# Performance work log

Measured on AMD Instinct MI355X. Metric: run time of the kernel, lower is better.

## Reference

```python
import jax, jax.numpy as jnp
import numpy as np

N = 50000      # nodes
E = 600000     # edges (avg degree 12)
D_IN = 16      # node_input_size
D = 128        # hidden_size
H = 4          # num_heads
DH = D // H
L = 4          # message_passing_num
D_FF = 512     # 4*hidden FFN expansion
D_OUT = 3      # output_size


def setup_inputs() -> dict:
    key = jax.random.key(0)
    ks = iter(jax.random.split(key, 32))
    def w(shape, fan_in):
        return jax.random.normal(next(ks), shape, jnp.float32) / np.float32(np.sqrt(fan_in))
    return {
        "features": jax.random.normal(next(ks), (N, D_IN), jnp.float32),
        "senders": jax.random.randint(next(ks), (E,), 0, N),
        "receivers": jax.random.randint(next(ks), (E,), 0, N),
        "enc_w1": w((D_IN, D), D_IN), "enc_b1": jnp.zeros((D,), jnp.float32),
        "enc_w2": w((D, D), D),       "enc_b2": jnp.zeros((D,), jnp.float32),
        "wq": w((L, D, D), D), "wk": w((L, D, D), D),
        "wv": w((L, D, D), D), "wo": w((L, D, D), D),
        "ln1_s": jnp.ones((L, D), jnp.float32), "ln1_b": jnp.zeros((L, D), jnp.float32),
        "ffn_w1": w((L, D, D_FF), D), "ffn_b1": jnp.zeros((L, D_FF), jnp.float32),
        "ffn_w2": w((L, D_FF, D), D_FF), "ffn_b2": jnp.zeros((L, D), jnp.float32),
        "ln2_s": jnp.ones((L, D), jnp.float32), "ln2_b": jnp.zeros((L, D), jnp.float32),
        "dec_w1": w((D, D_OUT), D), "dec_b1": jnp.zeros((D_OUT,), jnp.float32),
        "dec_w2": w((D_OUT, D_OUT), D_OUT), "dec_b2": jnp.zeros((D_OUT,), jnp.float32),
    }


def _ln(x, s, b):
    mu = x.mean(-1, keepdims=True)
    var = ((x - mu) ** 2).mean(-1, keepdims=True)
    return (x - mu) * jax.lax.rsqrt(var + 1e-5) * s + b


def _graph_mha(x, senders, receivers, wq, wk, wv, wo):
    # Adjacency-masked attention done sparsely over the edge list
    # (equivalent to softmax over the BCOO adjacency pattern).
    n = x.shape[0]
    q = (x @ wq).reshape(n, H, DH)
    k = (x @ wk).reshape(n, H, DH)
    v = (x @ wv).reshape(n, H, DH)
    scores = (q[receivers] * k[senders]).sum(-1) / np.float32(np.sqrt(DH))  # [E,H]
    m = jax.ops.segment_max(scores, receivers, num_segments=n)             # [N,H]
    m = jnp.where(jnp.isfinite(m), m, 0.0)
    a = jnp.exp(scores - m[receivers])                                      # [E,H]
    denom = jax.ops.segment_sum(a, receivers, num_segments=n)              # [N,H]
    msg = jax.ops.segment_sum(a[:, :, None] * v[senders], receivers, num_segments=n)  # [N,H,DH]
    out = (msg / (denom[:, :, None] + 1e-9)).reshape(n, D)
    return out @ wo


def reference(features, senders, receivers,
              enc_w1, enc_b1, enc_w2, enc_b2,
              wq, wk, wv, wo, ln1_s, ln1_b,
              ffn_w1, ffn_b1, ffn_w2, ffn_b2, ln2_s, ln2_b,
              dec_w1, dec_b1, dec_w2, dec_b2):
    # encode
    x = jnp.maximum(features @ enc_w1 + enc_b1, 0.0) @ enc_w2 + enc_b2     # [N,D]
    # process: L pre-LN sparse-attention transformer blocks
    for l in range(L):
        h = _ln(x, ln1_s[l], ln1_b[l])
        x = x + _graph_mha(h, senders, receivers, wq[l], wk[l], wv[l], wo[l])
        h = _ln(x, ln2_s[l], ln2_b[l])
        x = x + jnp.maximum(h @ ffn_w1[l] + ffn_b1[l], 0.0) @ ffn_w2[l] + ffn_b2[l]
    # decode
    return jnp.maximum(x @ dec_w1 + dec_b1, 0.0) @ dec_w2 + dec_b2         # [N,D_OUT]
```

## Files before the change

### kernel.cpp

```cpp
#include <hip/hip_runtime.h>
#include <hip/hip_bf16.h>
#include <math.h>

#define D     128
#define NHEAD 4
#define DH    32
#define DFF   512
#define DIN   16
#define MAXDEG 64
#define TN    16

typedef __attribute__((ext_vector_type(8))) short bf16x8;
typedef __attribute__((ext_vector_type(4))) float f32x4;
typedef __hip_bfloat16 bf16;

#define QSCALE_L2E 0.2550348838f

#define AP 132
#define BM 64

__global__ void k_zero_int(int* p, int n) {
    int i = blockIdx.x * blockDim.x + threadIdx.x;
    if (i < n) p[i] = 0;
}

__global__ void k_fill(const int* __restrict__ recv, const int* __restrict__ senders,
                       int* __restrict__ deg, int* __restrict__ eid, int E) {
    int e = blockIdx.x * blockDim.x + threadIdx.x;
    if (e >= E) return;
    int r = recv[e];
    int pos = atomicAdd(&deg[r], 1);
    if (pos < MAXDEG) eid[r * MAXDEG + pos] = senders[e];
}

__global__ void k_wt(const float* __restrict__ wq, const float* __restrict__ wk,
                     const float* __restrict__ wv, const float* __restrict__ wo,
                     const float* __restrict__ w1, const float* __restrict__ w2,
                     const float* __restrict__ encw2,
                     bf16* __restrict__ wqkvT, bf16* __restrict__ woT,
                     bf16* __restrict__ w1T, bf16* __restrict__ w2T,
                     bf16* __restrict__ encw2T) {
    int r = blockIdx.y;
    const float* src; bf16* dst; int K, Nout;
    if (r < 12) {
        int l = r / 3, sel = r % 3;
        src = (sel == 0 ? wq : sel == 1 ? wk : wv) + (size_t)l * D * D;
        dst = wqkvT + (size_t)l * 3 * D * D + (size_t)sel * D * D;
        K = D; Nout = D;
    } else if (r < 16) {
        int l = r - 12;
        src = wo + (size_t)l * D * D; dst = woT + (size_t)l * D * D; K = D; Nout = D;
    } else if (r < 20) {
        int l = r - 16;
        src = w1 + (size_t)l * D * DFF; dst = w1T + (size_t)l * D * DFF; K = D; Nout = DFF;
    } else if (r < 24) {
        int l = r - 20;
        src = w2 + (size_t)l * DFF * D; dst = w2T + (size_t)l * DFF * D; K = DFF; Nout = D;
    } else {
        src = encw2; dst = encw2T; K = D; Nout = D;
    }
    int total = K * Nout;
    int i = blockIdx.x * blockDim.x + threadIdx.x;
    if (i >= total) return;
    int k = i / Nout, j = i % Nout;
    dst[(size_t)j * K + k] = __float2bfloat16(src[i]);
}

__device__ __forceinline__ void load_afrag(const bf16* A, int arow, int quad,
                                           int N, bf16x8* afr) {
    const bf16* ab = A + (size_t)arow * D + quad * 8;
#pragma unroll
    for (int i = 0; i < 4; i++) {
        uint4 v = make_uint4(0u, 0u, 0u, 0u);
        if (arow < N) v = *(const uint4*)(ab + i * 32);
        afr[i] = *(bf16x8*)&v;
    }
}

template<int OP>
__global__ __launch_bounds__(256) void k_gemm(
        const bf16* __restrict__ A, const bf16* __restrict__ Bt,
        const float* __restrict__ bias,
        const float* __restrict__ lns, const float* __restrict__ lnb,
        float* x, bf16* outB, int N) {
    __shared__ alignas(16) bf16 Wsm[128][AP];
    int m0 = blockIdx.x * BM;
    int t = threadIdx.x;
    int wave = t >> 6, lane = t & 63;
    int quad = lane >> 4, l16 = lane & 15;
    int wm = wave * 16;

    bf16x8 afr[4];
    load_afrag(A, m0 + wm + l16, quad, N, afr);
#pragma unroll
    for (int it = 0; it < 8; it++) {
        int ci = it * 256 + t;
        int rr = ci >> 4, cc = (ci & 15) * 8;
        *(uint4*)&Wsm[rr][cc] = *(const uint4*)(Bt + (size_t)rr * D + cc);
    }
    __syncthreads();

    f32x4 acc[8];
#pragma unroll
    for (int j = 0; j < 8; j++) acc[j] = (f32x4){0.f, 0.f, 0.f, 0.f};
#pragma unroll
    for (int i = 0; i < 4; i++) {
#pragma unroll
        for (int j = 0; j < 8; j++) {
            bf16x8 bfr = *(const bf16x8*)&Wsm[j * 16 + l16][i * 32 + quad * 8];
            acc[j] = __builtin_amdgcn_mfma_f32_16x16x32_bf16(afr[i], bfr, acc[j], 0, 0, 0);
        }
    }

    int rowb = m0 + wm + quad * 4;
    float bv[8];
    if (OP == 5) {
#pragma unroll
        for (int j = 0; j < 8; j++) bv[j] = bias[j * 16 + l16];
    }
#pragma unroll
    for (int j = 0; j < 8; j++) {
        int col = j * 16 + l16;
#pragma unroll
        for (int r = 0; r < 4; r++) {
            int gr = rowb + r;
            if (gr >= N) continue;
            float val = acc[j][r];
            if (OP == 5) val += bv[j];
            if (OP == 2) val += x[(size_t)gr * D + col];
            acc[j][r] = val;
        }
    }
    float lsv[8], lbv[8];
#pragma unroll
    for (int j = 0; j < 8; j++) {
        lsv[j] = lns[j * 16 + l16];
        lbv[j] = lnb[j * 16 + l16];
    }
#pragma unroll
    for (int r = 0; r < 4; r++) {
        float s1 = 0.f, s2 = 0.f;
#pragma unroll
        for (int j = 0; j < 8; j++) {
            float v = acc[j][r];
            s1 += v; s2 += v * v;
        }
        s1 += __shfl_xor(s1, 1, 64);  s2 += __shfl_xor(s2, 1, 64);
        s1 += __shfl_xor(s1, 2, 64);  s2 += __shfl_xor(s2, 2, 64);
        s1 += __shfl_xor(s1, 4, 64);  s2 += __shfl_xor(s2, 4, 64);
        s1 += __shfl_xor(s1, 8, 64);  s2 += __shfl_xor(s2, 8, 64);
        float mu = s1 * (1.f / 128.f);
        float var = s2 * (1.f / 128.f) - mu * mu;
        float rinv = rsqrtf(fmaxf(var, 0.f) + 1e-5f);
        int gr = rowb + r;
        if (gr >= N) continue;
#pragma unroll
        for (int j = 0; j < 8; j++) {
            int col = j * 16 + l16;
            float v = acc[j][r];
            x[(size_t)gr * D + col] = v;
            outB[(size_t)gr * D + col] =
                __float2bfloat16((v - mu) * rinv * lsv[j] + lbv[j]);
        }
    }
}

__global__ __launch_bounds__(256) void k_qkv(
        const bf16* __restrict__ hb, const bf16* __restrict__ wqkvT,
        bf16* __restrict__ qb, bf16* __restrict__ kvb, int N) {
    __shared__ alignas(16) bf16 Wsm[128][AP];
    int m0 = blockIdx.x * BM;
    int t = threadIdx.x;
    int wave = t >> 6, lane = t & 63;
    int quad = lane >> 4, l16 = lane & 15;
    int wm = wave * 16;

    bf16x8 afr[4];
    load_afrag(hb, m0 + wm + l16, quad, N, afr);

    for (int y = 0; y < 3; y++) {
        const bf16* W = wqkvT + (size_t)y * D * D;
#pragma unroll
        for (int it = 0; it < 8; it++) {
            int ci = it * 256 + t;
            int rr = ci >> 4, cc = (ci & 15) * 8;
            *(uint4*)&Wsm[rr][cc] = *(const uint4*)(W + (size_t)rr * D + cc);
        }
        __syncthreads();

        f32x4 acc[8];
#pragma unroll
        for (int j = 0; j < 8; j++) acc[j] = (f32x4){0.f, 0.f, 0.f, 0.f};
#pragma unroll
        for (int i = 0; i < 4; i++) {
#pragma unroll
            for (int j = 0; j < 8; j++) {
                bf16x8 bfr = *(const bf16x8*)&Wsm[j * 16 + l16][i * 32 + quad * 8];
                acc[j] = __builtin_amdgcn_mfma_f32_16x16x32_bf16(afr[i], bfr, acc[j], 0, 0, 0);
            }
        }
        int rowb = m0 + wm + quad * 4;
#pragma unroll
        for (int j = 0; j < 8; j++) {
            int col = j * 16 + l16;
#pragma unroll
            for (int r = 0; r < 4; r++) {
                int gr = rowb + r;
                if (gr >= N) continue;
                float val = acc[j][r];
                if (y == 0) qb[(size_t)gr * D + col] = __float2bfloat16(val * QSCALE_L2E);
                else kvb[((size_t)gr * D + col) * 2 + (y - 1)] = __float2bfloat16(val);
            }
        }
        if (y < 2) __syncthreads();
    }
}

template<bool DOLN>
__global__ __launch_bounds__(256) void k_ffn(
        const bf16* __restrict__ hb, const bf16* __restrict__ w1T,
        const float* __restrict__ b1,
        const bf16* __restrict__ w2T, const float* __restrict__ b2,
        const float* __restrict__ lns, const float* __restrict__ lnb,
        float* x, bf16* outB, int N) {
    __shared__ alignas(16) bf16 Wsm[128][AP];
    __shared__ alignas(16) bf16 Hsm[64][AP];
    int m0 = blockIdx.x * 64;
    int t = threadIdx.x;
    int wave = t >> 6, lane = t & 63;
    int quad = lane >> 4, l16 = lane & 15;
    int wm = wave * 16;

    bf16x8 afr[4];
    load_afrag(hb, m0 + wm + l16, quad, N, afr);
#pragma unroll
    for (int it = 0; it < 8; it++) {
        int ci = it * 256 + t;
        int rr = ci >> 4, cc = (ci & 15) * 8;
        *(uint4*)&Wsm[rr][cc] = *(const uint4*)(w1T + (size_t)rr * D + cc);
    }
    __syncthreads();

    f32x4 acc2[8];
#pragma unroll
    for (int j = 0; j < 8; j++) acc2[j] = (f32x4){0.f, 0.f, 0.f, 0.f};

    for (int c = 0; c < 4; c++) {
        f32x4 accP[8];
#pragma unroll
        for (int j = 0; j < 8; j++) accP[j] = (f32x4){0.f, 0.f, 0.f, 0.f};
#pragma unroll
        for (int i = 0; i < 4; i++) {
#pragma unroll
            for (int j = 0; j < 8; j++) {
                bf16x8 bfr = *(const bf16x8*)&Wsm[j * 16 + l16][i * 32 + quad * 8];
                accP[j] = __builtin_amdgcn_mfma_f32_16x16x32_bf16(afr[i], bfr, accP[j], 0, 0, 0);
            }
        }
        __syncthreads();
#pragma unroll
        for (int it = 0; it < 8; it++) {
            int ci = it * 256 + t;
            int rr = ci >> 4, cc = (ci & 15) * 8;
            *(uint4*)&Wsm[rr][cc] = *(const uint4*)(w2T + (size_t)rr * DFF + c * 128 + cc);
        }
        {
            float bv[8];
#pragma unroll
            for (int j = 0; j < 8; j++) bv[j] = b1[c * 128 + j * 16 + l16];
            int rw = wm + quad * 4;
#pragma unroll
            for (int j = 0; j < 8; j++) {
                int col = j * 16 + l16;
#pragma unroll
                for (int r = 0; r < 4; r++)
                    Hsm[rw + r][col] = __float2bfloat16(fmaxf(accP[j][r] + bv[j], 0.f));
            }
        }
        __syncthreads();
#pragma unroll
        for (int ks = 0; ks < 4; ks++) {
            bf16x8 af2 = *(const bf16x8*)&Hsm[wm + l16][ks * 32 + quad * 8];
#pragma unroll
            for (int j = 0; j < 8; j++) {
                bf16x8 bfr = *(const bf16x8*)&Wsm[j * 16 + l16][ks * 32 + quad * 8];
                acc2[j] = __builtin_amdgcn_mfma_f32_16x16x32_bf16(af2, bfr, acc2[j], 0, 0, 0);
            }
        }
        if (c < 3) {
            __syncthreads();
#pragma unroll
            for (int it = 0; it < 8; it++) {
                int ci = it * 256 + t;
                int rr = ci >> 4, cc = (ci & 15) * 8;
                *(uint4*)&Wsm[rr][cc] =
                    *(const uint4*)(w1T + (size_t)((c + 1) * 128 + rr) * D + cc);
            }
            __syncthreads();
        }
    }

    int rowb = m0 + wm + quad * 4;
    float bv[8];
#pragma unroll
    for (int j = 0; j < 8; j++) bv[j] = b2[j * 16 + l16];
#pragma unroll
    for (int j = 0; j < 8; j++) {
        int col = j * 16 + l16;
#pragma unroll
        for (int r = 0; r < 4; r++) {
            int gr = rowb + r;
            if (gr >= N) continue;
            acc2[j][r] += bv[j] + x[(size_t)gr * D + col];
        }
    }
    if (!DOLN) {
#pragma unroll
        for (int j = 0; j < 8; j++) {
            int col = j * 16 + l16;
#pragma unroll
            for (int r = 0; r < 4; r++) {
                int gr = rowb + r;
                if (gr < N) x[(size_t)gr * D + col] = acc2[j][r];
            }
        }
        return;
    }
    float lsv[8], lbv[8];
#pragma unroll
    for (int j = 0; j < 8; j++) {
        lsv[j] = lns[j * 16 + l16];
        lbv[j] = lnb[j * 16 + l16];
    }
#pragma unroll
    for (int r = 0; r < 4; r++) {
        float s1 = 0.f, s2 = 0.f;
#pragma unroll
        for (int j = 0; j < 8; j++) {
            float v = acc2[j][r];
            s1 += v; s2 += v * v;
        }
        s1 += __shfl_xor(s1, 1, 64);  s2 += __shfl_xor(s2, 1, 64);
        s1 += __shfl_xor(s1, 2, 64);  s2 += __shfl_xor(s2, 2, 64);
        s1 += __shfl_xor(s1, 4, 64);  s2 += __shfl_xor(s2, 4, 64);
        s1 += __shfl_xor(s1, 8, 64);  s2 += __shfl_xor(s2, 8, 64);
        float mu = s1 * (1.f / 128.f);
        float var = s2 * (1.f / 128.f) - mu * mu;
        float rinv = rsqrtf(fmaxf(var, 0.f) + 1e-5f);
        int gr = rowb + r;
        if (gr >= N) continue;
#pragma unroll
        for (int j = 0; j < 8; j++) {
            int col = j * 16 + l16;
            float v = acc2[j][r];
            x[(size_t)gr * D + col] = v;
            outB[(size_t)gr * D + col] = __float2bfloat16((v - mu) * rinv * lsv[j] + lbv[j]);
        }
    }
}

__global__ void k_enc1(const float* __restrict__ feat,
                       const float* __restrict__ w1, const float* __restrict__ b1,
                       bf16* __restrict__ hb, int N) {
    __shared__ float fsh[TN][DIN];
    int n0 = blockIdx.x * TN;
    int j = threadIdx.x;
    int nvalid = min(TN, N - n0);
    for (int idx = j; idx < TN * DIN; idx += 128) {
        int n = idx / DIN, i = idx % DIN;
        fsh[n][i] = (n < nvalid) ? feat[(n0 + n) * DIN + i] : 0.f;
    }
    __syncthreads();
    float bb = b1[j];
#pragma unroll
    for (int n = 0; n < TN; n++) {
        float a = bb;
#pragma unroll
        for (int i = 0; i < DIN; i++) a += fsh[n][i] * w1[i * D + j];
        if (n < nvalid) hb[(size_t)(n0 + n) * D + j] = __float2bfloat16(fmaxf(a, 0.f));
    }
}

__global__ __launch_bounds__(128) void k_attn(
        const bf16* __restrict__ qb, const uint* __restrict__ kvb,
        const int* __restrict__ deg, const int* __restrict__ eid,
        bf16* __restrict__ out, int N) {
    __shared__ float sl[32], sa[32][4];
    int r = blockIdx.x;
    int t = threadIdx.x;
    int wave = t >> 6, lane = t & 63;
    int g = lane & 7;
    int h = (lane >> 3) & 3;
    int slot = wave * 2 + (lane >> 5);
    int d0 = h * 32 + g * 4;
    uint2 qw = *(const uint2*)(qb + (size_t)r * D + d0);
    float4 qv;
    qv.x = __uint_as_float(qw.x << 16);
    qv.y = __uint_as_float(qw.x & 0xFFFF0000u);
    qv.z = __uint_as_float(qw.y << 16);
    qv.w = __uint_as_float(qw.y & 0xFFFF0000u);
    int cnt = min(deg[r], MAXDEG);
    const int* row = eid + (size_t)r * MAXDEG;
    float l = 0.f, a0 = 0.f, a1 = 0.f, a2 = 0.f, a3 = 0.f;
    for (int base = 0; base < cnt; base += 8) {
        int eiA = base + slot, eiB = base + 4 + slot;
        bool vA = eiA < cnt, vB = eiB < cnt;
        int sA = vA ? row[eiA] : 0;
        int sB = vB ? row[eiB] : 0;
        uint4 wA = *(const uint4*)(kvb + (size_t)sA * D + d0);
        uint4 wB = *(const uint4*)(kvb + (size_t)sB * D + d0);
        {
            float k0 = __uint_as_float(wA.x << 16), v0 = __uint_as_float(wA.x & 0xFFFF0000u);
            float k1 = __uint_as_float(wA.y << 16), v1 = __uint_as_float(wA.y & 0xFFFF0000u);
            float k2 = __uint_as_float(wA.z << 16), v2 = __uint_as_float(wA.z & 0xFFFF0000u);
            float k3 = __uint_as_float(wA.w << 16), v3 = __uint_as_float(wA.w & 0xFFFF0000u);
            float p = qv.x * k0 + qv.y * k1 + qv.z * k2 + qv.w * k3;
            p += __shfl_xor(p, 1, 64);
            p += __shfl_xor(p, 2, 64);
            p += __shfl_xor(p, 4, 64);
            float e = vA ? exp2f(p) : 0.f;
            l += e;
            a0 += e * v0; a1 += e * v1; a2 += e * v2; a3 += e * v3;
        }
        {
            float k0 = __uint_as_float(wB.x << 16), v0 = __uint_as_float(wB.x & 0xFFFF0000u);
            float k1 = __uint_as_float(wB.y << 16), v1 = __uint_as_float(wB.y & 0xFFFF0000u);
            float k2 = __uint_as_float(wB.z << 16), v2 = __uint_as_float(wB.z & 0xFFFF0000u);
            float k3 = __uint_as_float(wB.w << 16), v3 = __uint_as_float(wB.w & 0xFFFF0000u);
            float p = qv.x * k0 + qv.y * k1 + qv.z * k2 + qv.w * k3;
            p += __shfl_xor(p, 1, 64);
            p += __shfl_xor(p, 2, 64);
            p += __shfl_xor(p, 4, 64);
            float e = vB ? exp2f(p) : 0.f;
            l += e;
            a0 += e * v0; a1 += e * v1; a2 += e * v2; a3 += e * v3;
        }
    }
    l  += __shfl_xor(l, 32, 64);
    a0 += __shfl_xor(a0, 32, 64);
    a1 += __shfl_xor(a1, 32, 64);
    a2 += __shfl_xor(a2, 32, 64);
    a3 += __shfl_xor(a3, 32, 64);
    if (wave == 1 && lane < 32) {
        sl[lane] = l;
        sa[lane][0] = a0; sa[lane][1] = a1; sa[lane][2] = a2; sa[lane][3] = a3;
    }
    __syncthreads();
    if (wave == 0 && lane < 32) {
        l += sl[lane];
        float inv = 1.f / (l + 1e-9f);
        bf16 o[4];
        o[0] = __float2bfloat16((a0 + sa[lane][0]) * inv);
        o[1] = __float2bfloat16((a1 + sa[lane][1]) * inv);
        o[2] = __float2bfloat16((a2 + sa[lane][2]) * inv);
        o[3] = __float2bfloat16((a3 + sa[lane][3]) * inv);
        *(uint2*)(out + (size_t)r * D + d0) = *(uint2*)o;
    }
}

__global__ void k_decode(const float* __restrict__ x,
                         const float* __restrict__ w1, const float* __restrict__ b1,
                         const float* __restrict__ w2, const float* __restrict__ b2,
                         float* __restrict__ out, int N) {
    int node = blockIdx.x * 4 + (threadIdx.x >> 6);
    int lane = threadIdx.x & 63;
    if (node >= N) return;
    float a0 = x[(size_t)node * D + lane], a1 = x[(size_t)node * D + lane + 64];
    float acc0 = a0 * w1[lane * 3 + 0] + a1 * w1[(lane + 64) * 3 + 0];
    float acc1 = a0 * w1[lane * 3 + 1] + a1 * w1[(lane + 64) * 3 + 1];
    float acc2 = a0 * w1[lane * 3 + 2] + a1 * w1[(lane + 64) * 3 + 2];
#pragma unroll
    for (int m = 32; m >= 1; m >>= 1) {
        acc0 += __shfl_xor(acc0, m, 64);
        acc1 += __shfl_xor(acc1, m, 64);
        acc2 += __shfl_xor(acc2, m, 64);
    }
    if (lane == 0) {
        float t0 = fmaxf(acc0 + b1[0], 0.f);
        float t1 = fmaxf(acc1 + b1[1], 0.f);
        float t2 = fmaxf(acc2 + b1[2], 0.f);
        for (int o = 0; o < 3; o++)
            out[(size_t)node * 3 + o] =
                t0 * w2[0 * 3 + o] + t1 * w2[1 * 3 + o] + t2 * w2[2 * 3 + o] + b2[o];
    }
}

extern "C" void kernel_launch(void* const* d_in, const int* in_sizes, int n_in,
                              void* d_out, int out_size, void* d_ws, size_t ws_size,
                              hipStream_t stream) {
    const float* feat    = (const float*)d_in[0];
    const int*   senders = (const int*)d_in[1];
    const int*   recv    = (const int*)d_in[2];
    const float* enc_w1  = (const float*)d_in[3];
    const float* enc_b1  = (const float*)d_in[4];
    const float* enc_w2  = (const float*)d_in[5];
    const float* enc_b2  = (const float*)d_in[6];
    const float* wq      = (const float*)d_in[7];
    const float* wk      = (const float*)d_in[8];
    const float* wv      = (const float*)d_in[9];
    const float* wo      = (const float*)d_in[10];
    const float* ln1_s   = (const float*)d_in[11];
    const float* ln1_b   = (const float*)d_in[12];
    const float* ffn_w1  = (const float*)d_in[13];
    const float* ffn_b1  = (const float*)d_in[14];
    const float* ffn_w2  = (const float*)d_in[15];
    const float* ffn_b2  = (const float*)d_in[16];
    const float* ln2_s   = (const float*)d_in[17];
    const float* ln2_b   = (const float*)d_in[18];
    const float* dec_w1  = (const float*)d_in[19];
    const float* dec_b1  = (const float*)d_in[20];
    const float* dec_w2  = (const float*)d_in[21];
    const float* dec_b2  = (const float*)d_in[22];

    int N = in_sizes[0] / DIN;
    int E = in_sizes[1];

    char* p = (char*)d_ws;
    float* x   = (float*)p;  p += (size_t)N * D * 4;
    bf16*  qb  = (bf16*)p;   p += (size_t)N * D * 2;
    bf16*  kvb = (bf16*)p;   p += (size_t)N * D * 2 * 2;
    bf16*  hb  = (bf16*)p;   p += (size_t)N * D * 2;
    int* deg   = (int*)p;    p += (size_t)N * 4;
    int* eid   = (int*)p;    p += (size_t)N * MAXDEG * 4;
    bf16* wqkvT  = (bf16*)p; p += (size_t)4 * 3 * D * D * 2;
    bf16* woT    = (bf16*)p; p += (size_t)4 * D * D * 2;
    bf16* w1T    = (bf16*)p; p += (size_t)4 * D * DFF * 2;
    bf16* w2T    = (bf16*)p; p += (size_t)4 * DFF * D * 2;
    bf16* encw2T = (bf16*)p; p += (size_t)D * D * 2;

    int gm = (N + BM - 1) / BM;

    k_wt<<<dim3(256, 25), 256, 0, stream>>>(wq, wk, wv, wo, ffn_w1, ffn_w2, enc_w2,
                                            wqkvT, woT, w1T, w2T, encw2T);
    k_zero_int<<<(N + 255) / 256, 256, 0, stream>>>(deg, N);
    k_fill<<<(E + 255) / 256, 256, 0, stream>>>(recv, senders, deg, eid, E);
    k_enc1<<<(N + TN - 1) / TN, 128, 0, stream>>>(feat, enc_w1, enc_b1, hb, N);
    k_gemm<5><<<gm, 256, 0, stream>>>(hb, encw2T, enc_b2, ln1_s, ln1_b, x, hb, N);

    for (int l = 0; l < 4; l++) {
        k_qkv<<<gm, 256, 0, stream>>>(hb, wqkvT + (size_t)l * 3 * D * D, qb, kvb, N);
        k_attn<<<N, 128, 0, stream>>>(qb, (const uint*)kvb, deg, eid, hb, N);
        k_gemm<2><<<gm, 256, 0, stream>>>(hb, woT + (size_t)l * D * D,
                                          nullptr, ln2_s + l * D, ln2_b + l * D,
                                          x, hb, N);
        if (l < 3)
            k_ffn<true><<<gm, 256, 0, stream>>>(hb, w1T + (size_t)l * D * DFF,
                                                ffn_b1 + l * DFF,
                                                w2T + (size_t)l * DFF * D, ffn_b2 + l * D,
                                                ln1_s + (l + 1) * D, ln1_b + (l + 1) * D,
                                                x, hb, N);
        else
            k_ffn<false><<<gm, 256, 0, stream>>>(hb, w1T + (size_t)l * D * DFF,
                                                 ffn_b1 + l * DFF,
                                                 w2T + (size_t)l * DFF * D, ffn_b2 + l * D,
                                                 nullptr, nullptr, x, nullptr, N);
    }
    k_decode<<<(N + 3) / 4, 256, 0, stream>>>(x, dec_w1, dec_b1, dec_w2, dec_b2,
                                              (float*)d_out, N);
}
```

Before: 761.0 us.

## Fuse output projection, residual and LN2 into the FFN kernel

Merges the attention output-projection GEMM (plus residual add and second LayerNorm) into the FFN kernel, so the post-attention residual stays in registers and the normalized activations go through shared memory instead of global memory. This removes one kernel launch per layer and one global write and read of x and hb per layer. In exchange the fused kernel holds an extra accumulator array in registers, which may reduce occupancy, and the encoder GEMM is specialized into its own non-template kernel.

```diff
diff --git a/kernel.cpp b/kernel.cpp
--- a/kernel.cpp
+++ b/kernel.cpp
@@ -77,8 +77,7 @@
     }
 }
 
-template<int OP>
-__global__ __launch_bounds__(256) void k_gemm(
+__global__ __launch_bounds__(256) void k_gemm5(
         const bf16* __restrict__ A, const bf16* __restrict__ Bt,
         const float* __restrict__ bias,
         const float* __restrict__ lns, const float* __restrict__ lnb,
@@ -113,30 +112,17 @@
     }
 
     int rowb = m0 + wm + quad * 4;
-    float bv[8];
-    if (OP == 5) {
-#pragma unroll
-        for (int j = 0; j < 8; j++) bv[j] = bias[j * 16 + l16];
-    }
+    float bv[8], lsv[8], lbv[8];
 #pragma unroll
     for (int j = 0; j < 8; j++) {
-        int col = j * 16 + l16;
-#pragma unroll
-        for (int r = 0; r < 4; r++) {
-            int gr = rowb + r;
-            if (gr >= N) continue;
-            float val = acc[j][r];
-            if (OP == 5) val += bv[j];
-            if (OP == 2) val += x[(size_t)gr * D + col];
-            acc[j][r] = val;
-        }
-    }
-    float lsv[8], lbv[8];
-#pragma unroll
-    for (int j = 0; j < 8; j++) {
+        bv[j]  = bias[j * 16 + l16];
         lsv[j] = lns[j * 16 + l16];
         lbv[j] = lnb[j * 16 + l16];
     }
+#pragma unroll
+    for (int j = 0; j < 8; j++)
+#pragma unroll
+        for (int r = 0; r < 4; r++) acc[j][r] += bv[j];
 #pragma unroll
     for (int r = 0; r < 4; r++) {
         float s1 = 0.f, s2 = 0.f;
@@ -217,9 +203,10 @@
 }
 
 template<bool DOLN>
-__global__ __launch_bounds__(256) void k_ffn(
-        const bf16* __restrict__ hb, const bf16* __restrict__ w1T,
-        const float* __restrict__ b1,
+__global__ __launch_bounds__(256) void k_wo_ffn(
+        const bf16* __restrict__ ha, const bf16* __restrict__ woT,
+        const float* __restrict__ ln2s, const float* __restrict__ ln2b,
+        const bf16* __restrict__ w1T, const float* __restrict__ b1,
         const bf16* __restrict__ w2T, const float* __restrict__ b2,
         const float* __restrict__ lns, const float* __restrict__ lnb,
         float* x, bf16* outB, int N) {
@@ -230,16 +217,82 @@
     int wave = t >> 6, lane = t & 63;
     int quad = lane >> 4, l16 = lane & 15;
     int wm = wave * 16;
+    int rowb = m0 + wm + quad * 4;
 
     bf16x8 afr[4];
-    load_afrag(hb, m0 + wm + l16, quad, N, afr);
+    load_afrag(ha, m0 + wm + l16, quad, N, afr);
+#pragma unroll
+    for (int it = 0; it < 8; it++) {
+        int ci = it * 256 + t;
+        int rr = ci >> 4, cc = (ci & 15) * 8;
+        *(uint4*)&Wsm[rr][cc] = *(const uint4*)(woT + (size_t)rr * D + cc);
+    }
+    __syncthreads();
+
+    f32x4 accW[8];
+#pragma unroll
+    for (int j = 0; j < 8; j++) accW[j] = (f32x4){0.f, 0.f, 0.f, 0.f};
+#pragma unroll
+    for (int i = 0; i < 4; i++) {
+#pragma unroll
+        for (int j = 0; j < 8; j++) {
+            bf16x8 bfr = *(const bf16x8*)&Wsm[j * 16 + l16][i * 32 + quad * 8];
+            accW[j] = __builtin_amdgcn_mfma_f32_16x16x32_bf16(afr[i], bfr, accW[j], 0, 0, 0);
+        }
+    }
+    __syncthreads();
+
 #pragma unroll
     for (int it = 0; it < 8; it++) {
         int ci = it * 256 + t;
         int rr = ci >> 4, cc = (ci & 15) * 8;
         *(uint4*)&Wsm[rr][cc] = *(const uint4*)(w1T + (size_t)rr * D + cc);
     }
+#pragma unroll
+    for (int j = 0; j < 8; j++) {
+        int col = j * 16 + l16;
+#pragma unroll
+        for (int r = 0; r < 4; r++) {
+            int gr = rowb + r;
+            if (gr < N) accW[j][r] += x[(size_t)gr * D + col];
+        }
+    }
+    {
+        float l2s[8], l2b[8];
+#pragma unroll
+        for (int j = 0; j < 8; j++) {
+            l2s[j] = ln2s[j * 16 + l16];
+            l2b[j] = ln2b[j * 16 + l16];
+        }
+#pragma unroll
+        for (int r = 0; r < 4; r++) {
+            float s1 = 0.f, s2 = 0.f;
+#pragma unroll
+            for (int j = 0; j < 8; j++) {
+                float v = accW[j][r];
+                s1 += v; s2 += v * v;
+            }
+            s1 += __shfl_xor(s1, 1, 64);  s2 += __shfl_xor(s2, 1, 64);
+            s1 += __shfl_xor(s1, 2, 64);  s2 += __shfl_xor(s2, 2, 64);
+            s1 += __shfl_xor(s1, 4, 64);  s2 += __shfl_xor(s2, 4, 64);
+            s1 += __shfl_xor(s1, 8, 64);  s2 += __shfl_xor(s2, 8, 64);
+            float mu = s1 * (1.f / 128.f);
+            float var = s2 * (1.f / 128.f) - mu * mu;
+            float rinv = rsqrtf(fmaxf(var, 0.f) + 1e-5f);
+            int rw = wm + quad * 4 + r;
+#pragma unroll
+            for (int j = 0; j < 8; j++) {
+                int col = j * 16 + l16;
+                Hsm[rw][col] = __float2bfloat16(
+                    (accW[j][r] - mu) * rinv * l2s[j] + l2b[j]);
+            }
+        }
+    }
     __syncthreads();
+
+#pragma unroll
+    for (int i = 0; i < 4; i++)
+        afr[i] = *(const bf16x8*)&Hsm[wm + l16][i * 32 + quad * 8];
 
     f32x4 acc2[8];
 #pragma unroll
@@ -300,20 +353,14 @@
         }
     }
 
-    int rowb = m0 + wm + quad * 4;
     float bv[8];
 #pragma unroll
     for (int j = 0; j < 8; j++) bv[j] = b2[j * 16 + l16];
 #pragma unroll
-    for (int j = 0; j < 8; j++) {
-        int col = j * 16 + l16;
-#pragma unroll
-        for (int r = 0; r < 4; r++) {
-            int gr = rowb + r;
-            if (gr >= N) continue;
-            acc2[j][r] += bv[j] + x[(size_t)gr * D + col];
-        }
-    }
+    for (int j = 0; j < 8; j++)
+#pragma unroll
+        for (int r = 0; r < 4; r++)
+            acc2[j][r] += accW[j][r] + bv[j];
     if (!DOLN) {
 #pragma unroll
         for (int j = 0; j < 8; j++) {
@@ -535,25 +582,23 @@
     k_zero_int<<<(N + 255) / 256, 256, 0, stream>>>(deg, N);
     k_fill<<<(E + 255) / 256, 256, 0, stream>>>(recv, senders, deg, eid, E);
     k_enc1<<<(N + TN - 1) / TN, 128, 0, stream>>>(feat, enc_w1, enc_b1, hb, N);
-    k_gemm<5><<<gm, 256, 0, stream>>>(hb, encw2T, enc_b2, ln1_s, ln1_b, x, hb, N);
+    k_gemm5<<<gm, 256, 0, stream>>>(hb, encw2T, enc_b2, ln1_s, ln1_b, x, hb, N);
 
     for (int l = 0; l < 4; l++) {
         k_qkv<<<gm, 256, 0, stream>>>(hb, wqkvT + (size_t)l * 3 * D * D, qb, kvb, N);
         k_attn<<<N, 128, 0, stream>>>(qb, (const uint*)kvb, deg, eid, hb, N);
-        k_gemm<2><<<gm, 256, 0, stream>>>(hb, woT + (size_t)l * D * D,
-                                          nullptr, ln2_s + l * D, ln2_b + l * D,
-                                          x, hb, N);
         if (l < 3)
-            k_ffn<true><<<gm, 256, 0, stream>>>(hb, w1T + (size_t)l * D * DFF,
-                                                ffn_b1 + l * DFF,
-                                                w2T + (size_t)l * DFF * D, ffn_b2 + l * D,
-                                                ln1_s + (l + 1) * D, ln1_b + (l + 1) * D,
-                                                x, hb, N);
+            k_wo_ffn<true><<<gm, 256, 0, stream>>>(
+                hb, woT + (size_t)l * D * D, ln2_s + l * D, ln2_b + l * D,
+                w1T + (size_t)l * D * DFF, ffn_b1 + l * DFF,
+                w2T + (size_t)l * DFF * D, ffn_b2 + l * D,
+                ln1_s + (l + 1) * D, ln1_b + (l + 1) * D, x, hb, N);
         else
-            k_ffn<false><<<gm, 256, 0, stream>>>(hb, w1T + (size_t)l * D * DFF,
-                                                 ffn_b1 + l * DFF,
-                                                 w2T + (size_t)l * DFF * D, ffn_b2 + l * D,
-                                                 nullptr, nullptr, x, nullptr, N);
+            k_wo_ffn<false><<<gm, 256, 0, stream>>>(
+                hb, woT + (size_t)l * D * D, ln2_s + l * D, ln2_b + l * D,
+                w1T + (size_t)l * D * DFF, ffn_b1 + l * DFF,
+                w2T + (size_t)l * DFF * D, ffn_b2 + l * D,
+                nullptr, nullptr, x, nullptr, N);
     }
     k_decode<<<(N + 3) / 4, 256, 0, stream>>>(x, dec_w1, dec_b1, dec_w2, dec_b2,
                                               (float*)d_out, N);
```

New measurement: 859.2 us. 12.9% more time.
